# Optimization experiments

Hardware: AMD Instinct MI355X
Metric: run time of the kernel (lower is better)

## Reference

```python
import jax, jax.numpy as jnp
import numpy as np

H, W = 256, 256
N = 512
BG = jnp.zeros(3, dtype=jnp.float32)  # background_color=(0,0,0)


def setup_inputs() -> dict:
    key = jax.random.key(0)
    k1, k2, k3, k4, k5 = jax.random.split(key, 5)
    # positions: xy in [-1.5,1.5], z in [2,6] so every gaussian passes the z>0.01 test
    xy = jax.random.uniform(k1, (N, 2), minval=-1.5, maxval=1.5, dtype=jnp.float32)
    zpos = jax.random.uniform(k2, (N, 1), minval=2.0, maxval=6.0, dtype=jnp.float32)
    positions = jnp.concatenate([xy, zpos], axis=-1)
    # PSD 3D covariances with ~0.05 world-space std
    A = 0.05 * jax.random.normal(k3, (N, 3, 3), dtype=jnp.float32)
    cov3d = A @ jnp.swapaxes(A, -1, -2) + 1e-6 * jnp.eye(3, dtype=jnp.float32)
    opacities = jax.random.uniform(k4, (N, 1), dtype=jnp.float32)
    colors = jax.random.uniform(k5, (N, 3), dtype=jnp.float32)
    K = jnp.array([[300.0, 0.0, 128.0], [0.0, 300.0, 128.0], [0.0, 0.0, 1.0]], dtype=jnp.float32)
    R = jnp.eye(3, dtype=jnp.float32)
    t = jnp.zeros(3, dtype=jnp.float32)
    return {"positions": positions, "cov3d": cov3d, "opacities": opacities,
            "colors": colors, "K": K, "R": R, "t": t}


def _render(positions, cov3d, opacities, colors, K, R, t):
    # --- project means to camera / image space ---
    means_cam = positions @ R.T + t                       # (N,3)
    z = means_cam[:, 2]                                   # all > 0.01 by construction
    proj = means_cam @ K.T                                # (N,3)
    means_2d = proj[:, :2] / proj[:, 2:3]                 # (N,2) pixel coords (x,y)

    # --- project 3D covariance to 2D: cov2d = J (R cov3d R^T) J^T + 0.3 I ---
    fx, fy = K[0, 0], K[1, 1]
    xc, yc = means_cam[:, 0], means_cam[:, 1]
    zero = jnp.zeros_like(z)
    J = jnp.stack([
        jnp.stack([fx / z, zero, -fx * xc / z**2], axis=-1),
        jnp.stack([zero, fy / z, -fy * yc / z**2], axis=-1),
    ], axis=1)                                            # (N,2,3)
    cov_cam = jnp.einsum('ij,njk,lk->nil', R, cov3d, R)   # (N,3,3)
    cov2d = jnp.einsum('nij,njk,nlk->nil', J, cov_cam, J) + 0.3 * jnp.eye(2, dtype=jnp.float32)

    # --- front-to-back depth sort ---
    order = jnp.argsort(z)
    means_2d = means_2d[order]
    cov2d = cov2d[order]
    opac = opacities[:, 0][order]
    cols = colors[order]

    # --- 2x2 inverse and 3-sigma radii ---
    a, b, c = cov2d[:, 0, 0], cov2d[:, 0, 1], cov2d[:, 1, 1]
    det = jnp.clip(a * c - b * b, 1e-8, None)
    inv00, inv01, inv11 = c / det, -b / det, a / det
    max_eig = (a + c) * 0.5 + jnp.sqrt(jnp.clip(((a - c) * 0.5) ** 2 + b ** 2, 1e-8, None))
    radii = 3.0 * jnp.sqrt(max_eig)

    # --- bounding boxes (int() truncates toward zero, as in torch) ---
    mx, my = means_2d[:, 0], means_2d[:, 1]
    x_min = jnp.maximum(0.0, jnp.trunc(mx - radii))
    x_max = jnp.minimum(float(W), jnp.trunc(mx + radii) + 1.0)
    y_min = jnp.maximum(0.0, jnp.trunc(my - radii))
    y_max = jnp.minimum(float(H), jnp.trunc(my + radii) + 1.0)

    xs = jnp.arange(W, dtype=jnp.float32)
    ys = jnp.arange(H, dtype=jnp.float32)
    dx = xs[None, :] - mx[:, None]                        # (N,W)
    dy = ys[None, :] - my[:, None]                        # (N,H)
    mask_x = (xs[None, :] >= x_min[:, None]) & (xs[None, :] < x_max[:, None])
    mask_y = (ys[None, :] >= y_min[:, None]) & (ys[None, :] < y_max[:, None])
    mask = (mask_y[:, :, None] & mask_x[:, None, :]).astype(jnp.float32)  # (N,H,W)

    # --- gaussian weights on the grid ---
    mahal = (inv00[:, None, None] * dx[:, None, :] ** 2
             + 2.0 * inv01[:, None, None] * dy[:, :, None] * dx[:, None, :]
             + inv11[:, None, None] * dy[:, :, None] ** 2)                 # (N,H,W)
    alpha = opac[:, None, None] * jnp.exp(-0.5 * mahal) * mask            # (N,H,W)

    # --- front-to-back alpha compositing ---
    # sequential: contrib_i = alpha_i * (1 - alpha_acc_{i-1}); alpha_acc_i += contrib_i
    # closed form: T_i = prod_{j<i} (1 - alpha_j)  (exclusive cumprod)
    T = jnp.concatenate([jnp.ones((1, H, W), dtype=alpha.dtype),
                         jnp.cumprod(1.0 - alpha, axis=0)[:-1]], axis=0)
    contrib = alpha * T                                                   # (N,H,W)
    image = BG[None, None, :] + jnp.einsum('nhw,nc->hwc', contrib, cols)  # (H,W,3)
    return image


def reference(positions, cov3d, opacities, colors, K, R, t):
    return _render(positions, cov3d, opacities, colors, K, R, t)
```

## Files before the change

kernel.cpp:

```cpp
#include <hip/hip_runtime.h>


constexpr int IMG_H = 256;
constexpr int IMG_W = 256;
constexpr int MAXN  = 512;
constexpr int TW    = 16;
constexpr int TH    = 16;
constexpr int NTHR  = TW * TH;

__global__ __launch_bounds__(NTHR) void fused_raster_kernel(
    const float* __restrict__ positions,
    const float* __restrict__ cov3d,
    const float* __restrict__ opacities,
    const float* __restrict__ colors,
    const float* __restrict__ Km,
    const float* __restrict__ Rm,
    const float* __restrict__ tv,
    float* __restrict__ out)
{
    __shared__ float4 s_srt[(MAXN + 4) * 3];
    __shared__ unsigned long long s_key[MAXN];
    __shared__ int s_total;

    const int tid = threadIdx.y * TW + threadIdx.x;
    if (tid == 0) s_total = 0;

    const int tx0i = blockIdx.x * TW;
    const int ty0i = blockIdx.y * TH;
    const float tx0 = (float)tx0i;
    const float ty0 = (float)ty0i;

    const float R00 = Rm[0], R01 = Rm[1], R02 = Rm[2];
    const float R10 = Rm[3], R11 = Rm[4], R12 = Rm[5];
    const float R20 = Rm[6], R21 = Rm[7], R22 = Rm[8];
    const float t0 = tv[0], t1 = tv[1], t2 = tv[2];
    const float K00 = Km[0], K01 = Km[1], K02 = Km[2];
    const float K10 = Km[3], K11 = Km[4], K12 = Km[5];
    const float K20 = Km[6], K21 = Km[7], K22 = Km[8];
    const float fx = K00, fy = K11;

    __syncthreads();

    float r_mx[2], r_my[2], r_h00[2], r_h01[2], r_h11[2];
    float r_op[2], r_cr[2], r_cg[2], r_cb[2];
    float r_xmin[2], r_xmax[2], r_ymin[2], r_ymax[2];
    unsigned long long r_key[2];
    bool r_hit[2];

    #pragma unroll
    for (int k = 0; k < 2; ++k) {
        const int g = k * NTHR + tid;

        const float px = positions[g*3+0];
        const float py = positions[g*3+1];
        const float pz = positions[g*3+2];

        const float cx = R00*px + R01*py + R02*pz + t0;
        const float cy = R10*px + R11*py + R12*pz + t1;
        const float cz = R20*px + R21*py + R22*pz + t2;

        const float pr0 = K00*cx + K01*cy + K02*cz;
        const float pr1 = K10*cx + K11*cy + K12*cz;
        const float pr2 = K20*cx + K21*cy + K22*cz;
        const float mx = pr0 / pr2;
        const float my = pr1 / pr2;

        const float invz  = 1.0f / cz;
        const float invz2 = invz * invz;
        const float j00 =  fx * invz;
        const float j02 = -fx * cx * invz2;
        const float j11 =  fy * invz;
        const float j12 = -fy * cy * invz2;

        const float C00 = cov3d[g*9+0], C01 = cov3d[g*9+1], C02 = cov3d[g*9+2];
        const float C10 = cov3d[g*9+3], C11 = cov3d[g*9+4], C12 = cov3d[g*9+5];
        const float C20 = cov3d[g*9+6], C21 = cov3d[g*9+7], C22 = cov3d[g*9+8];

        const float T100 = R00*C00 + R01*C10 + R02*C20;
        const float T101 = R00*C01 + R01*C11 + R02*C21;
        const float T102 = R00*C02 + R01*C12 + R02*C22;
        const float T110 = R10*C00 + R11*C10 + R12*C20;
        const float T111 = R10*C01 + R11*C11 + R12*C21;
        const float T112 = R10*C02 + R11*C12 + R12*C22;
        const float T120 = R20*C00 + R21*C10 + R22*C20;
        const float T121 = R20*C01 + R21*C11 + R22*C21;
        const float T122 = R20*C02 + R21*C12 + R22*C22;
        const float M00 = T100*R00 + T101*R01 + T102*R02;
        const float M01 = T100*R10 + T101*R11 + T102*R12;
        const float M02 = T100*R20 + T101*R21 + T102*R22;
        const float M11 = T110*R10 + T111*R11 + T112*R12;
        const float M12 = T110*R20 + T111*R21 + T112*R22;
        const float M20 = T120*R00 + T121*R01 + T122*R02;
        const float M21 = T120*R10 + T121*R11 + T122*R12;
        const float M22 = T120*R20 + T121*R21 + T122*R22;

        const float v00 = M00*j00 + M02*j02;
        const float v02 = M20*j00 + M22*j02;
        const float v10 = M01*j11 + M02*j12;
        const float v11 = M11*j11 + M12*j12;
        const float v12 = M21*j11 + M22*j12;

        const float va = j00*v00 + j02*v02 + 0.3f;
        const float vb = j00*v10 + j02*v12;
        const float vc = j11*v11 + j12*v12 + 0.3f;

        const float det  = fmaxf(va*vc - vb*vb, 1e-8f);
        const float idet = 1.0f / det;
        const float inv00 =  vc * idet;
        const float inv01 = -vb * idet;
        const float inv11 =  va * idet;

        const float half_diff = (va - vc) * 0.5f;
        const float disc = fmaxf(half_diff*half_diff + vb*vb, 1e-8f);
        const float max_eig = (va + vc) * 0.5f + sqrtf(disc);
        const float radii = 3.0f * sqrtf(max_eig);

        const float x_min = fmaxf(0.0f, truncf(mx - radii));
        const float x_max = fminf((float)IMG_W, truncf(mx + radii) + 1.0f);
        const float y_min = fmaxf(0.0f, truncf(my - radii));
        const float y_max = fminf((float)IMG_H, truncf(my + radii) + 1.0f);

        r_mx[k] = mx;  r_my[k] = my;
        r_h00[k] = -0.5f*inv00;  r_h01[k] = -inv01;  r_h11[k] = -0.5f*inv11;
        r_op[k] = opacities[g];
        r_cr[k] = colors[g*3+0]; r_cg[k] = colors[g*3+1]; r_cb[k] = colors[g*3+2];
        r_xmin[k] = x_min; r_xmax[k] = x_max;
        r_ymin[k] = y_min; r_ymax[k] = y_max;

        r_key[k] = ((unsigned long long)__float_as_uint(cz) << 32) | (unsigned)g;

        const bool hit = (x_min < tx0 + (float)TW) && (x_max > tx0) &&
                         (y_min < ty0 + (float)TH) && (y_max > ty0);
        r_hit[k] = hit;
        if (hit) {
            const int pos = atomicAdd(&s_total, 1);
            s_key[pos] = r_key[k];
        }
    }
    __syncthreads();
    const int K = s_total;

    int rank0 = 0, rank1 = 0;
    for (int j = 0; j < K; ++j) {
        const unsigned long long kj = s_key[j];
        rank0 += (kj < r_key[0]) ? 1 : 0;
        rank1 += (kj < r_key[1]) ? 1 : 0;
    }

    #pragma unroll
    for (int k = 0; k < 2; ++k) {
        if (r_hit[k]) {
            const int xm = max(0,  (int)r_xmin[k] - tx0i);
            const int xM = min(TW, (int)r_xmax[k] - tx0i);
            const int ym = max(0,  (int)r_ymin[k] - ty0i);
            const int yM = min(TH, (int)r_ymax[k] - ty0i);
            const unsigned pk = (unsigned)xm | ((unsigned)xM << 5)
                              | ((unsigned)ym << 10) | ((unsigned)yM << 15);
            const int rk = (k == 0) ? rank0 : rank1;
            s_srt[rk*3+0] = make_float4(r_mx[k], r_my[k], r_h00[k], r_h01[k]);
            s_srt[rk*3+1] = make_float4(r_h11[k], r_op[k], r_cr[k], r_cg[k]);
            s_srt[rk*3+2] = make_float4(r_cb[k], __uint_as_float(pk), 0.0f, 0.0f);
        }
    }
    if (tid < 6) s_srt[K*3 + tid] = make_float4(0.0f, 0.0f, 0.0f, 0.0f);
    __syncthreads();

    const int tix = threadIdx.x, tiy = threadIdx.y;
    const float fxp = (float)(tx0i + tix);
    const float fyp = (float)(ty0i + tiy);

    float T = 1.0f, accr = 0.0f, accg = 0.0f, accb = 0.0f;

    float4 A0 = s_srt[0], A1 = s_srt[1], A2 = s_srt[2];
    float4 B0 = s_srt[3], B1 = s_srt[4], B2 = s_srt[5];

    for (int m = 0; m < K; m += 2) {
        const int pf = (m + 2) * 3;
        const float4 C0 = s_srt[pf+0], C1 = s_srt[pf+1], C2 = s_srt[pf+2];
        const float4 D0 = s_srt[pf+3], D1 = s_srt[pf+4], D2 = s_srt[pf+5];

        {
            const unsigned pk = __float_as_uint(A2.y);
            const bool in = (tix >= (int)(pk & 31u)) & (tix < (int)((pk >> 5) & 31u))
                          & (tiy >= (int)((pk >> 10) & 31u)) & (tiy < (int)((pk >> 15) & 31u));
            const float dx = fxp - A0.x;
            const float dy = fyp - A0.y;
            const float e = A0.z*dx*dx + A0.w*dx*dy + A1.x*dy*dy;
            const float a = in ? A1.y * __expf(e) : 0.0f;
            const float w = T * a;
            accr = fmaf(w, A1.z, accr);
            accg = fmaf(w, A1.w, accg);
            accb = fmaf(w, A2.x, accb);
            T *= (1.0f - a);
        }
        {
            const unsigned pk = __float_as_uint(B2.y);
            const bool in = (tix >= (int)(pk & 31u)) & (tix < (int)((pk >> 5) & 31u))
                          & (tiy >= (int)((pk >> 10) & 31u)) & (tiy < (int)((pk >> 15) & 31u));
            const float dx = fxp - B0.x;
            const float dy = fyp - B0.y;
            const float e = B0.z*dx*dx + B0.w*dx*dy + B1.x*dy*dy;
            const float a = in ? B1.y * __expf(e) : 0.0f;
            const float w = T * a;
            accr = fmaf(w, B1.z, accr);
            accg = fmaf(w, B1.w, accg);
            accb = fmaf(w, B2.x, accb);
            T *= (1.0f - a);
        }

        A0 = C0; A1 = C1; A2 = C2;
        B0 = D0; B1 = D1; B2 = D2;

        if (!__any(T > 1.0e-5f)) break;
    }

    const int pix = ((ty0i + tiy) * IMG_W + (tx0i + tix)) * 3;
    out[pix + 0] = accr;
    out[pix + 1] = accg;
    out[pix + 2] = accb;
}

extern "C" void kernel_launch(void* const* d_in, const int* in_sizes, int n_in,
                              void* d_out, int out_size, void* d_ws, size_t ws_size,
                              hipStream_t stream)
{
    const float* positions = (const float*)d_in[0];
    const float* cov3d     = (const float*)d_in[1];
    const float* opacities = (const float*)d_in[2];
    const float* colors    = (const float*)d_in[3];
    const float* Km        = (const float*)d_in[4];
    const float* Rm        = (const float*)d_in[5];
    const float* tv        = (const float*)d_in[6];
    float* out = (float*)d_out;

    dim3 block(TW, TH);
    dim3 grid(IMG_W / TW, IMG_H / TH);
    fused_raster_kernel<<<grid, block, 0, stream>>>(
        positions, cov3d, opacities, colors, Km, Rm, tv, out);
}
```

Before: 76.39 us.

## Split gaussian list across two thread halves per pixel and merge transmittance

Doubles the block to 512 threads, so each thread preprocesses exactly one gaussian, and the two 256-thread halves composite the first and second halves of the depth-sorted list for the same 16x16 pixel tile. The back half's colour and transmittance are combined through shared memory as front + T_front * back, which shortens the serial compositing chain per thread. Compaction into the hit list now uses a wavefront ballot with one atomic per wave instead of one atomic per gaussian. In exchange, the back half cannot stop early on the front half's saturation, and the extra sync and shared buffer cost a little occupancy.

```diff
diff --git a/kernel.cpp b/kernel.cpp
--- a/kernel.cpp
+++ b/kernel.cpp
@@ -6,7 +6,7 @@
 constexpr int MAXN  = 512;
 constexpr int TW    = 16;
 constexpr int TH    = 16;
-constexpr int NTHR  = TW * TH;
+constexpr int NTHR  = 512;
 
 __global__ __launch_bounds__(NTHR) void fused_raster_kernel(
     const float* __restrict__ positions,
@@ -20,9 +20,16 @@
 {
     __shared__ float4 s_srt[(MAXN + 4) * 3];
     __shared__ unsigned long long s_key[MAXN];
+    __shared__ float4 s_comb[TW * TH];
     __shared__ int s_total;
 
-    const int tid = threadIdx.y * TW + threadIdx.x;
+    const int tix  = threadIdx.x;
+    const int ty   = threadIdx.y;
+    const int tid  = ty * TW + tix;
+    const int lane = tid & 63;
+    const int half = ty >> 4;
+    const int py   = ty & 15;
+
     if (tid == 0) s_total = 0;
 
     const int tx0i = blockIdx.x * TW;
@@ -41,140 +48,132 @@
 
     __syncthreads();
 
-    float r_mx[2], r_my[2], r_h00[2], r_h01[2], r_h11[2];
-    float r_op[2], r_cr[2], r_cg[2], r_cb[2];
-    float r_xmin[2], r_xmax[2], r_ymin[2], r_ymax[2];
-    unsigned long long r_key[2];
-    bool r_hit[2];
-
-    #pragma unroll
-    for (int k = 0; k < 2; ++k) {
-        const int g = k * NTHR + tid;
-
-        const float px = positions[g*3+0];
-        const float py = positions[g*3+1];
-        const float pz = positions[g*3+2];
-
-        const float cx = R00*px + R01*py + R02*pz + t0;
-        const float cy = R10*px + R11*py + R12*pz + t1;
-        const float cz = R20*px + R21*py + R22*pz + t2;
-
-        const float pr0 = K00*cx + K01*cy + K02*cz;
-        const float pr1 = K10*cx + K11*cy + K12*cz;
-        const float pr2 = K20*cx + K21*cy + K22*cz;
-        const float mx = pr0 / pr2;
-        const float my = pr1 / pr2;
-
-        const float invz  = 1.0f / cz;
-        const float invz2 = invz * invz;
-        const float j00 =  fx * invz;
-        const float j02 = -fx * cx * invz2;
-        const float j11 =  fy * invz;
-        const float j12 = -fy * cy * invz2;
-
-        const float C00 = cov3d[g*9+0], C01 = cov3d[g*9+1], C02 = cov3d[g*9+2];
-        const float C10 = cov3d[g*9+3], C11 = cov3d[g*9+4], C12 = cov3d[g*9+5];
-        const float C20 = cov3d[g*9+6], C21 = cov3d[g*9+7], C22 = cov3d[g*9+8];
-
-        const float T100 = R00*C00 + R01*C10 + R02*C20;
-        const float T101 = R00*C01 + R01*C11 + R02*C21;
-        const float T102 = R00*C02 + R01*C12 + R02*C22;
-        const float T110 = R10*C00 + R11*C10 + R12*C20;
-        const float T111 = R10*C01 + R11*C11 + R12*C21;
-        const float T112 = R10*C02 + R11*C12 + R12*C22;
-        const float T120 = R20*C00 + R21*C10 + R22*C20;
-        const float T121 = R20*C01 + R21*C11 + R22*C21;
-        const float T122 = R20*C02 + R21*C12 + R22*C22;
-        const float M00 = T100*R00 + T101*R01 + T102*R02;
-        const float M01 = T100*R10 + T101*R11 + T102*R12;
-        const float M02 = T100*R20 + T101*R21 + T102*R22;
-        const float M11 = T110*R10 + T111*R11 + T112*R12;
-        const float M12 = T110*R20 + T111*R21 + T112*R22;
-        const float M20 = T120*R00 + T121*R01 + T122*R02;
-        const float M21 = T120*R10 + T121*R11 + T122*R12;
-        const float M22 = T120*R20 + T121*R21 + T122*R22;
-
-        const float v00 = M00*j00 + M02*j02;
-        const float v02 = M20*j00 + M22*j02;
-        const float v10 = M01*j11 + M02*j12;
-        const float v11 = M11*j11 + M12*j12;
-        const float v12 = M21*j11 + M22*j12;
-
-        const float va = j00*v00 + j02*v02 + 0.3f;
-        const float vb = j00*v10 + j02*v12;
-        const float vc = j11*v11 + j12*v12 + 0.3f;
-
-        const float det  = fmaxf(va*vc - vb*vb, 1e-8f);
-        const float idet = 1.0f / det;
-        const float inv00 =  vc * idet;
-        const float inv01 = -vb * idet;
-        const float inv11 =  va * idet;
-
-        const float half_diff = (va - vc) * 0.5f;
-        const float disc = fmaxf(half_diff*half_diff + vb*vb, 1e-8f);
-        const float max_eig = (va + vc) * 0.5f + sqrtf(disc);
-        const float radii = 3.0f * sqrtf(max_eig);
-
-        const float x_min = fmaxf(0.0f, truncf(mx - radii));
-        const float x_max = fminf((float)IMG_W, truncf(mx + radii) + 1.0f);
-        const float y_min = fmaxf(0.0f, truncf(my - radii));
-        const float y_max = fminf((float)IMG_H, truncf(my + radii) + 1.0f);
-
-        r_mx[k] = mx;  r_my[k] = my;
-        r_h00[k] = -0.5f*inv00;  r_h01[k] = -inv01;  r_h11[k] = -0.5f*inv11;
-        r_op[k] = opacities[g];
-        r_cr[k] = colors[g*3+0]; r_cg[k] = colors[g*3+1]; r_cb[k] = colors[g*3+2];
-        r_xmin[k] = x_min; r_xmax[k] = x_max;
-        r_ymin[k] = y_min; r_ymax[k] = y_max;
-
-        r_key[k] = ((unsigned long long)__float_as_uint(cz) << 32) | (unsigned)g;
-
-        const bool hit = (x_min < tx0 + (float)TW) && (x_max > tx0) &&
-                         (y_min < ty0 + (float)TH) && (y_max > ty0);
-        r_hit[k] = hit;
+    const int g = tid;
+
+    const float px = positions[g*3+0];
+    const float py3 = positions[g*3+1];
+    const float pz = positions[g*3+2];
+
+    const float cx = R00*px + R01*py3 + R02*pz + t0;
+    const float cy = R10*px + R11*py3 + R12*pz + t1;
+    const float cz = R20*px + R21*py3 + R22*pz + t2;
+
+    const float pr0 = K00*cx + K01*cy + K02*cz;
+    const float pr1 = K10*cx + K11*cy + K12*cz;
+    const float pr2 = K20*cx + K21*cy + K22*cz;
+    const float mx = pr0 / pr2;
+    const float my = pr1 / pr2;
+
+    const float invz  = 1.0f / cz;
+    const float invz2 = invz * invz;
+    const float j00 =  fx * invz;
+    const float j02 = -fx * cx * invz2;
+    const float j11 =  fy * invz;
+    const float j12 = -fy * cy * invz2;
+
+    const float C00 = cov3d[g*9+0], C01 = cov3d[g*9+1], C02 = cov3d[g*9+2];
+    const float C10 = cov3d[g*9+3], C11 = cov3d[g*9+4], C12 = cov3d[g*9+5];
+    const float C20 = cov3d[g*9+6], C21 = cov3d[g*9+7], C22 = cov3d[g*9+8];
+
+    const float T100 = R00*C00 + R01*C10 + R02*C20;
+    const float T101 = R00*C01 + R01*C11 + R02*C21;
+    const float T102 = R00*C02 + R01*C12 + R02*C22;
+    const float T110 = R10*C00 + R11*C10 + R12*C20;
+    const float T111 = R10*C01 + R11*C11 + R12*C21;
+    const float T112 = R10*C02 + R11*C12 + R12*C22;
+    const float T120 = R20*C00 + R21*C10 + R22*C20;
+    const float T121 = R20*C01 + R21*C11 + R22*C21;
+    const float T122 = R20*C02 + R21*C12 + R22*C22;
+    const float M00 = T100*R00 + T101*R01 + T102*R02;
+    const float M01 = T100*R10 + T101*R11 + T102*R12;
+    const float M02 = T100*R20 + T101*R21 + T102*R22;
+    const float M11 = T110*R10 + T111*R11 + T112*R12;
+    const float M12 = T110*R20 + T111*R21 + T112*R22;
+    const float M20 = T120*R00 + T121*R01 + T122*R02;
+    const float M21 = T120*R10 + T121*R11 + T122*R12;
+    const float M22 = T120*R20 + T121*R21 + T122*R22;
+
+    const float v00 = M00*j00 + M02*j02;
+    const float v02 = M20*j00 + M22*j02;
+    const float v10 = M01*j11 + M02*j12;
+    const float v11 = M11*j11 + M12*j12;
+    const float v12 = M21*j11 + M22*j12;
+
+    const float va = j00*v00 + j02*v02 + 0.3f;
+    const float vb = j00*v10 + j02*v12;
+    const float vc = j11*v11 + j12*v12 + 0.3f;
+
+    const float det  = fmaxf(va*vc - vb*vb, 1e-8f);
+    const float idet = 1.0f / det;
+    const float inv00 =  vc * idet;
+    const float inv01 = -vb * idet;
+    const float inv11 =  va * idet;
+
+    const float half_diff = (va - vc) * 0.5f;
+    const float disc = fmaxf(half_diff*half_diff + vb*vb, 1e-8f);
+    const float max_eig = (va + vc) * 0.5f + sqrtf(disc);
+    const float radii = 3.0f * sqrtf(max_eig);
+
+    const float x_min = fmaxf(0.0f, truncf(mx - radii));
+    const float x_max = fminf((float)IMG_W, truncf(mx + radii) + 1.0f);
+    const float y_min = fmaxf(0.0f, truncf(my - radii));
+    const float y_max = fminf((float)IMG_H, truncf(my + radii) + 1.0f);
+
+    const unsigned long long key =
+        ((unsigned long long)__float_as_uint(cz) << 32) | (unsigned)g;
+
+    const bool hit = (x_min < tx0 + (float)TW) && (x_max > tx0) &&
+                     (y_min < ty0 + (float)TH) && (y_max > ty0);
+
+    {
+        const unsigned long long mb = __ballot(hit);
+        int base = 0;
+        if (lane == 0 && mb) base = atomicAdd(&s_total, __popcll(mb));
+        base = __shfl(base, 0);
         if (hit) {
-            const int pos = atomicAdd(&s_total, 1);
-            s_key[pos] = r_key[k];
+            const int pos = base + __popcll(mb & ((1ull << lane) - 1ull));
+            s_key[pos] = key;
         }
     }
     __syncthreads();
     const int K = s_total;
 
-    int rank0 = 0, rank1 = 0;
-    for (int j = 0; j < K; ++j) {
-        const unsigned long long kj = s_key[j];
-        rank0 += (kj < r_key[0]) ? 1 : 0;
-        rank1 += (kj < r_key[1]) ? 1 : 0;
-    }
-
-    #pragma unroll
-    for (int k = 0; k < 2; ++k) {
-        if (r_hit[k]) {
-            const int xm = max(0,  (int)r_xmin[k] - tx0i);
-            const int xM = min(TW, (int)r_xmax[k] - tx0i);
-            const int ym = max(0,  (int)r_ymin[k] - ty0i);
-            const int yM = min(TH, (int)r_ymax[k] - ty0i);
-            const unsigned pk = (unsigned)xm | ((unsigned)xM << 5)
-                              | ((unsigned)ym << 10) | ((unsigned)yM << 15);
-            const int rk = (k == 0) ? rank0 : rank1;
-            s_srt[rk*3+0] = make_float4(r_mx[k], r_my[k], r_h00[k], r_h01[k]);
-            s_srt[rk*3+1] = make_float4(r_h11[k], r_op[k], r_cr[k], r_cg[k]);
-            s_srt[rk*3+2] = make_float4(r_cb[k], __uint_as_float(pk), 0.0f, 0.0f);
-        }
+    int rank = 0;
+    for (int j = 0; j < K; ++j)
+        rank += (s_key[j] < key) ? 1 : 0;
+
+    if (hit) {
+        const int xm = max(0,  (int)x_min - tx0i);
+        const int xM = min(TW, (int)x_max - tx0i);
+        const int ym = max(0,  (int)y_min - ty0i);
+        const int yM = min(TH, (int)y_max - ty0i);
+        const unsigned pk = (unsigned)xm | ((unsigned)xM << 5)
+                          | ((unsigned)ym << 10) | ((unsigned)yM << 15);
+        s_srt[rank*3+0] = make_float4(mx, my, -0.5f*inv00, -inv01);
+        s_srt[rank*3+1] = make_float4(-0.5f*inv11, opacities[g],
+                                      colors[g*3+0], colors[g*3+1]);
+        s_srt[rank*3+2] = make_float4(colors[g*3+2], __uint_as_float(pk),
+                                      0.0f, 0.0f);
     }
     if (tid < 6) s_srt[K*3 + tid] = make_float4(0.0f, 0.0f, 0.0f, 0.0f);
     __syncthreads();
 
-    const int tix = threadIdx.x, tiy = threadIdx.y;
+    int Kf = (K + 1) >> 1;
+    Kf += (Kf & 1);
+    if (Kf > K) Kf = K + (K & 1);
+    const int mStart = half ? Kf : 0;
+    const int mEnd   = half ? K  : Kf;
+
     const float fxp = (float)(tx0i + tix);
-    const float fyp = (float)(ty0i + tiy);
+    const float fyp = (float)(ty0i + py);
 
     float T = 1.0f, accr = 0.0f, accg = 0.0f, accb = 0.0f;
 
-    float4 A0 = s_srt[0], A1 = s_srt[1], A2 = s_srt[2];
-    float4 B0 = s_srt[3], B1 = s_srt[4], B2 = s_srt[5];
-
-    for (int m = 0; m < K; m += 2) {
+    const int sb = mStart * 3;
+    float4 A0 = s_srt[sb+0], A1 = s_srt[sb+1], A2 = s_srt[sb+2];
+    float4 B0 = s_srt[sb+3], B1 = s_srt[sb+4], B2 = s_srt[sb+5];
+
+    for (int m = mStart; m < mEnd; m += 2) {
         const int pf = (m + 2) * 3;
         const float4 C0 = s_srt[pf+0], C1 = s_srt[pf+1], C2 = s_srt[pf+2];
         const float4 D0 = s_srt[pf+3], D1 = s_srt[pf+4], D2 = s_srt[pf+5];
@@ -182,7 +181,7 @@
         {
             const unsigned pk = __float_as_uint(A2.y);
             const bool in = (tix >= (int)(pk & 31u)) & (tix < (int)((pk >> 5) & 31u))
-                          & (tiy >= (int)((pk >> 10) & 31u)) & (tiy < (int)((pk >> 15) & 31u));
+                          & (py >= (int)((pk >> 10) & 31u)) & (py < (int)((pk >> 15) & 31u));
             const float dx = fxp - A0.x;
             const float dy = fyp - A0.y;
             const float e = A0.z*dx*dx + A0.w*dx*dy + A1.x*dy*dy;
@@ -196,7 +195,7 @@
         {
             const unsigned pk = __float_as_uint(B2.y);
             const bool in = (tix >= (int)(pk & 31u)) & (tix < (int)((pk >> 5) & 31u))
-                          & (tiy >= (int)((pk >> 10) & 31u)) & (tiy < (int)((pk >> 15) & 31u));
+                          & (py >= (int)((pk >> 10) & 31u)) & (py < (int)((pk >> 15) & 31u));
             const float dx = fxp - B0.x;
             const float dy = fyp - B0.y;
             const float e = B0.z*dx*dx + B0.w*dx*dy + B1.x*dy*dy;
@@ -214,10 +213,18 @@
         if (!__any(T > 1.0e-5f)) break;
     }
 
-    const int pix = ((ty0i + tiy) * IMG_W + (tx0i + tix)) * 3;
-    out[pix + 0] = accr;
-    out[pix + 1] = accg;
-    out[pix + 2] = accb;
+    if (half == 1) s_comb[py * TW + tix] = make_float4(accr, accg, accb, T);
+    __syncthreads();
+    if (half == 0) {
+        const float4 b = s_comb[py * TW + tix];
+        accr = fmaf(T, b.x, accr);
+        accg = fmaf(T, b.y, accg);
+        accb = fmaf(T, b.z, accb);
+        const int pix = ((ty0i + py) * IMG_W + (tx0i + tix)) * 3;
+        out[pix + 0] = accr;
+        out[pix + 1] = accg;
+        out[pix + 2] = accb;
+    }
 }
 
 extern "C" void kernel_launch(void* const* d_in, const int* in_sizes, int n_in,
@@ -233,7 +240,7 @@
     const float* tv        = (const float*)d_in[6];
     float* out = (float*)d_out;
 
-    dim3 block(TW, TH);
+    dim3 block(TW, 2 * TH);
     dim3 grid(IMG_W / TW, IMG_H / TH);
     fused_raster_kernel<<<grid, block, 0, stream>>>(
         positions, cov3d, opacities, colors, Km, Rm, tv, out);
```

Result: faster. 72.17 us (-5.5%).
